# Optimization experiments

Hardware: AMD Instinct MI355X
Metric: run time of the kernel (lower is better)

The kernel has to match this reference:

```python
import jax, jax.numpy as jnp
import numpy as np

B, S, D, M = 8, 128, 512, 4
DEPTH, THR, TEMP, EPS = 16, 0.9999, 1.0, 1e-6


def setup_inputs() -> dict:
    key = jax.random.key(0)
    ks = jax.random.split(key, 13)
    def nrm(k, shape):
        return jax.random.normal(k, shape, jnp.float32) / np.sqrt(shape[-1]).astype(np.float32)
    return dict(
        x_real=jax.random.normal(ks[0], (B, S, D), jnp.float32),
        x_imag=jax.random.normal(ks[1], (B, S, D), jnp.float32),
        Wq_r=nrm(ks[2], (M, D, D)), Wq_i=nrm(ks[3], (M, D, D)),
        Wk_r=nrm(ks[4], (M, D, D)), Wk_i=nrm(ks[5], (M, D, D)),
        Wv_r=nrm(ks[6], (M, D, D)), Wv_i=nrm(ks[7], (M, D, D)),
        mod_bias=jnp.zeros((M, D), jnp.float32),
        ln_scale=jnp.ones((M, D), jnp.float32),
        ln_shift=jnp.zeros((M, D), jnp.float32),
        w_sal=nrm(ks[8], (M, 2 * D)),
        gru_Wih=nrm(ks[9], (2 * D, 3 * D)),
        gru_Whh=nrm(ks[10], (D, 3 * D)),
        gru_bih=jnp.zeros((3 * D,), jnp.float32),
        gru_bhh=jnp.zeros((3 * D,), jnp.float32),
        bias_W=nrm(ks[11], (D, M)),
        bias_b=jnp.zeros((M,), jnp.float32),
        w_halt=nrm(ks[12], (2 * D,)),
        b_halt=jnp.zeros((1,), jnp.float32),
    )


def reference(x_real, x_imag, Wq_r, Wq_i, Wk_r, Wk_i, Wv_r, Wv_i,
              mod_bias, ln_scale, ln_shift, w_sal,
              gru_Wih, gru_Whh, gru_bih, gru_bhh,
              bias_W, bias_b, w_halt, b_halt):
    scale = D ** -0.5

    def clin(xr, xi, Wr, Wi):
        # ComplexLinear broadcast over module axis: x [B,S,D], W [M,D,D] -> [M,B,S,D]
        rr = jnp.einsum('bsd,mde->mbse', xr, Wr)
        ii = jnp.einsum('bsd,mde->mbse', xi, Wi)
        ri = jnp.einsum('bsd,mde->mbse', xr, Wi)
        ir = jnp.einsum('bsd,mde->mbse', xi, Wr)
        return rr - ii, ri + ir

    def modules(zr, zi):
        # all M processor modules in parallel: ComplexAttention -> ModReLU -> ComplexLayerNorm
        qr, qi = clin(zr, zi, Wq_r, Wq_i)
        kr, ki = clin(zr, zi, Wk_r, Wk_i)
        vr, vi = clin(zr, zi, Wv_r, Wv_i)
        qf = jnp.concatenate([qr, qi], -1)            # [M,B,S,2D]
        kf = jnp.concatenate([kr, ki], -1)
        attn = jax.nn.softmax(jnp.einsum('mbsd,mbtd->mbst', qf, kf) * scale, -1)
        or_ = jnp.einsum('mbst,mbtd->mbsd', attn, vr)
        oi_ = jnp.einsum('mbst,mbtd->mbsd', attn, vi)
        # ModReLU
        mag = jnp.sqrt(or_ ** 2 + oi_ ** 2) + EPS
        g = jax.nn.relu(mag + mod_bias[:, None, None, :]) / mag
        or_, oi_ = or_ * g, oi_ * g
        # ComplexLayerNorm (normalize magnitude, keep phase; torch var is unbiased)
        mag = jnp.sqrt(or_ ** 2 + oi_ ** 2) + EPS
        mu = mag.mean(-1, keepdims=True)
        var = jnp.var(mag, axis=-1, keepdims=True, ddof=1)
        nm = (mag - mu) / jnp.sqrt(var + EPS)
        nm = nm * ln_scale[:, None, None, :] + ln_shift[:, None, None, :]
        ph = jnp.arctan2(oi_, or_)
        return nm * jnp.cos(ph), nm * jnp.sin(ph)

    def gru(xf, h):
        gx = xf @ gru_Wih + gru_bih
        gh = h @ gru_Whh + gru_bhh
        xr_, xz_, xn_ = jnp.split(gx, 3, -1)
        hr_, hz_, hn_ = jnp.split(gh, 3, -1)
        r = jax.nn.sigmoid(xr_ + hr_)
        zg = jax.nn.sigmoid(xz_ + hz_)
        n = jnp.tanh(xn_ + r * hn_)
        return (1.0 - zg) * n + zg * h

    def step(carry, _):
        zr, zi, h, cum, ar, ai, pond = carry
        pooled = jnp.concatenate([zr.mean(1), zi.mean(1)], -1)   # [B,2D]
        h = gru(pooled, h)                                       # ExecutiveController
        mbias = h @ bias_W + bias_b                              # [B,M]
        mr, mi = modules(zr, zi)                                 # [M,B,S,D]
        feat = jnp.concatenate([mr.mean(2), mi.mean(2)], -1)     # [M,B,2D]
        sal = jnp.einsum('mbf,mf->mb', feat, w_sal)              # salience
        w = jax.nn.softmax((sal + mbias.T) / TEMP, axis=0)       # module competition
        gr = jnp.einsum('mb,mbsd->bsd', w, mr)                   # global workspace broadcast
        gi = jnp.einsum('mb,mbsd->bsd', w, mi)
        gwp = jnp.concatenate([gr.mean(1), gi.mean(1)], -1)
        p = jax.nn.sigmoid(gwp @ w_halt + b_halt[0])             # [B] halting prob
        still = (cum < THR).astype(p.dtype)
        new_halt = ((cum + p) >= THR) & (cum < THR)
        wt = jnp.where(new_halt, 1.0 - cum, p) * still           # ACT weights
        cum = cum + wt
        ar = ar + wt[:, None, None] * gr
        ai = ai + wt[:, None, None] * gi
        pond = pond + still
        return (gr, gi, h, cum, ar, ai, pond), None

    z0 = jnp.zeros((B,), x_real.dtype)
    init = (x_real, x_imag, jnp.zeros((B, D), x_real.dtype), z0,
            jnp.zeros_like(x_real), jnp.zeros_like(x_imag), z0)
    (zr, zi, h, cum, ar, ai, pond), _ = jax.lax.scan(step, init, None, length=DEPTH)
    return jnp.stack([ar, ai])  # [2,B,S,D] accumulated workspace (real, imag)
```

## Files before the change

kernel.cpp:

```cpp
#include <hip/hip_runtime.h>
#include <math.h>

#define B 8
#define S 128
#define D 512
#define M 4
#define BS 1024
#define BSD 524288
#define DEPTH 16
#define THRESH 0.9999f
#define EPS 1e-6f
#define SCALE 0.04419417382415922f

typedef float floatx4 __attribute__((ext_vector_type(4)));
typedef short s8v __attribute__((ext_vector_type(8)));
typedef unsigned short us4 __attribute__((ext_vector_type(4)));

__device__ __forceinline__ unsigned short f2bf(float f) {
  unsigned int u = __float_as_uint(f);
  u += 0x7FFFu + ((u >> 16) & 1u);
  return (unsigned short)(u >> 16);
}
__device__ __forceinline__ float bf2f(unsigned short h) {
  return __uint_as_float((unsigned int)h << 16);
// ... 45 lines not shown
  ((float4*)(ws + OFF_ZI))[i4] = b;
  float4 z = {0.f, 0.f, 0.f, 0.f};
  ((float4*)(ws + OFF_AR))[i4] = z;
  ((float4*)(ws + OFF_AI))[i4] = z;
  int row = i4 >> 7;
  int d4 = (i4 & 127) * 4;
  float av[4] = {a.x, a.y, a.z, a.w}, bv[4] = {b.x, b.y, b.z, b.w};
  us4 hh, hl;
#pragma unroll
  for (int j = 0; j < 4; ++j) {
    unsigned short h = f2bf(av[j]); hh[j] = h; hl[j] = f2bf(av[j] - bf2f(h));
  }
  *(us4*)(xh + (size_t)row * 1024 + d4) = hh;
  *(us4*)(xl + (size_t)row * 1024 + d4) = hl;
#pragma unroll
  for (int j = 0; j < 4; ++j) {
    unsigned short h = f2bf(bv[j]); hh[j] = h; hl[j] = f2bf(bv[j] - bf2f(h));
  }
  *(us4*)(xh + (size_t)row * 1024 + 512 + d4) = hh;
  *(us4*)(xl + (size_t)row * 1024 + 512 + d4) = hl;
  if (i4 < (B * D) / 4) {
    ((float4*)(ws + OFF_H0))[i4] = z;
    ((float4*)(ws + OFF_H1))[i4] = z;
  }
  if (i4 < 16384) ((float4*)(ws + OFF_FEAT))[i4] = z;
  if (i4 < 2048)  ((float4*)(ws + OFF_GWP))[i4] = z;
  if (i4 < B) { ws[OFF_CUM + i4] = 0.f; ws[OFF_CUM2 + i4] = 0.f; }
}

__global__ __launch_bounds__(256) void k_wprep(const float* __restrict__ Wqr,
                                               const float* __restrict__ Wqi,
                                               const float* __restrict__ Wkr,
                                               const float* __restrict__ Wki,
                                               const float* __restrict__ Wvr,
                                               const float* __restrict__ Wvi,
                                               float* __restrict__ ws) {
  __shared__ float lt[64][65];
  unsigned short* wh = (unsigned short*)(ws + OFF_WH);
  unsigned short* wl = (unsigned short*)(ws + OFF_WL);
  int z = blockIdx.z, m = z / 6, idx = z % 6;
  const float* Wsrc;
  switch (idx) {
    case 0:  Wsrc = Wqr; break;
    case 1:  Wsrc = Wqi; break;
    case 2:  Wsrc = Wkr; break;
    case 3:  Wsrc = Wki; break;
    case 4:  Wsrc = Wvr; break;
    default: Wsrc = Wvi; break;
  }
  Wsrc += (size_t)m * D * D;
  int k0 = blockIdx.x * 64, n0 = blockIdx.y * 64;
  int tx = threadIdx.x & 63, ty = threadIdx.x >> 6;
#pragma unroll
  for (int i = 0; i < 16; ++i) {
    int kl = ty + i * 4;
    lt[kl][tx] = Wsrc[(size_t)(k0 + kl) * D + n0 + tx];
  }
  __syncthreads();
  unsigned short* whp = wh + (size_t)z * 262144;
  unsigned short* wlp = wl + (size_t)z * 262144;
#pragma unroll
  for (int i = 0; i < 16; ++i) {
    int nl = ty + i * 4;
    float v = lt[tx][nl];
    unsigned short h = f2bf(v);
    whp[(size_t)(n0 + nl) * 512 + k0 + tx] = h;
    wlp[(size_t)(n0 + nl) * 512 + k0 + tx] = f2bf(v - bf2f(h));
  }
}

__global__ __launch_bounds__(256) void k_gwp(const float* __restrict__ zr,
                                             const float* __restrict__ zi,
                                             float* __restrict__ gwp) {
  int idx = blockIdx.x * 256 + threadIdx.x;
  int b = idx >> 10;
  int f = idx & 1023;
  const float* src = (f < D) ? (zr + b * S * D + f) : (zi + b * S * D + (f - D));
  float s = 0.f;
#pragma unroll 8
  for (int ss = 0; ss < S; ++ss) s += src[ss * D];
  gwp[idx] = s * (1.0f / S);
}

__global__ __launch_bounds__(256) void k_qk(float* __restrict__ ws) {
  __shared__ __align__(16) unsigned short Ah[128 * 32], Al[128 * 32];
  __shared__ __align__(16) unsigned short Bh[128 * 32], Bl[128 * 32];
  int t = threadIdx.x;
  if (blockIdx.x == 0 && blockIdx.y == 0 && blockIdx.z == 0) {
    float4 z4 = {0.f, 0.f, 0.f, 0.f};
    for (int i = t; i < 4096; i += 256) ((float4*)(ws + OFF_PART))[i] = z4;
  }
  const unsigned short* xh = (const unsigned short*)(ws + OFF_XH);
  const unsigned short* xl = (const unsigned short*)(ws + OFF_XL);
  const unsigned short* wh = (const unsigned short*)(ws + OFF_WH);
  const unsigned short* wl = (const unsigned short*)(ws + OFF_WL);
  int z = blockIdx.z, m = z >> 2, w6 = z & 3;
  int pair = (w6 >> 1) * 2;
  int p1 = m * 6 + pair + (w6 & 1);
  int p2 = m * 6 + pair + ((w6 & 1) ^ 1);
  bool neg2 = ((w6 & 1) == 0);
  const unsigned short* PH1 = wh + (size_t)p1 * 262144;
  const unsigned short* PL1 = wl + (size_t)p1 * 262144;
  const unsigned short* PH2 = wh + (size_t)p2 * 262144;
  const unsigned short* PL2 = wl + (size_t)p2 * 262144;

  int row0 = blockIdx.y * 128;
  int col0 = blockIdx.x * 128;
  int lane = t & 63, w = t >> 6;
  int wr = w >> 1, wc = w & 1;
  int q = lane >> 4, r = lane & 15;
  int srow = t >> 2;
  int skoff = (t & 3) * 8;
  size_t wrow1 = (size_t)(col0 + srow) * 512 + skoff;
  size_t wrow2 = (size_t)(col0 + 64 + srow) * 512 + skoff;
  size_t xrow1 = (size_t)(row0 + srow) * 1024 + skoff;
  size_t xrow2 = (size_t)(row0 + 64 + srow) * 1024 + skoff;
  const s8v sgn = {(short)0x8000, (short)0x8000, (short)0x8000, (short)0x8000,
                   (short)0x8000, (short)0x8000, (short)0x8000, (short)0x8000};

  floatx4 acc[4][4];
#pragma unroll
  for (int i = 0; i < 4; ++i)
#pragma unroll
    for (int j = 0; j < 4; ++j) acc[i][j] = (floatx4){0.f, 0.f, 0.f, 0.f};

  for (int k0 = 0; k0 < 1024; k0 += 32) {
    const unsigned short *WgH, *WgL;
    int kk = k0;
    bool xon = false;
    if (k0 < 512) { WgH = PH1; WgL = PL1; }
    else          { WgH = PH2; WgL = PL2; kk = k0 - 512; xon = neg2; }
    gll16(xh + xrow1 + k0, (char*)Ah + t * 16);
    gll16(xh + xrow2 + k0, (char*)Ah + 4096 + t * 16);
    gll16(xl + xrow1 + k0, (char*)Al + t * 16);
    gll16(xl + xrow2 + k0, (char*)Al + 4096 + t * 16);
    gll16(WgH + wrow1 + kk, (char*)Bh + t * 16);
    gll16(WgH + wrow2 + kk, (char*)Bh + 4096 + t * 16);
    gll16(WgL + wrow1 + kk, (char*)Bl + t * 16);
    gll16(WgL + wrow2 + kk, (char*)Bl + 4096 + t * 16);
    __syncthreads();
    s8v ah[4], al[4], bh[4], bl[4];
#pragma unroll
    for (int i = 0; i < 4; ++i) {
      int ro = (wr * 64 + i * 16 + r) * 32 + q * 8;
      ah[i] = *(const s8v*)((const short*)Ah + ro);
      al[i] = *(const s8v*)((const short*)Al + ro);
    }
#pragma unroll
    for (int j = 0; j < 4; ++j) {
      int ro = (wc * 64 + j * 16 + r) * 32 + q * 8;
      bh[j] = *(const s8v*)((const short*)Bh + ro);
      bl[j] = *(const s8v*)((const short*)Bl + ro);
    }
    if (xon) {
#pragma unroll
      for (int j = 0; j < 4; ++j) { bh[j] = bh[j] ^ sgn; bl[j] = bl[j] ^ sgn; }
    }
#pragma unroll
    for (int i = 0; i < 4; ++i)
#pragma unroll
      for (int j = 0; j < 4; ++j) {
        acc[i][j] = __builtin_amdgcn_mfma_f32_16x16x32_bf16(ah[i], bh[j], acc[i][j], 0, 0, 0);
        acc[i][j] = __builtin_amdgcn_mfma_f32_16x16x32_bf16(ah[i], bl[j], acc[i][j], 0, 0, 0);
        acc[i][j] = __builtin_amdgcn_mfma_f32_16x16x32_bf16(al[i], bh[j], acc[i][j], 0, 0, 0);
      }
    __syncthreads();
  }
  unsigned short *dh, *dl;
  if (w6 < 2) { dh = (unsigned short*)(ws + OFF_QCH); dl = (unsigned short*)(ws + OFF_QCL); }
  else        { dh = (unsigned short*)(ws + OFF_KCH); dl = (unsigned short*)(ws + OFF_KCL); }
  int half = (w6 & 1) * 512;
  size_t base = (size_t)m * 1024 * 1024;
#pragma unroll
  for (int i = 0; i < 4; ++i)
#pragma unroll
    for (int j = 0; j < 4; ++j) {
      int rowb = row0 + wr * 64 + i * 16 + q * 4;
      int colb = col0 + wc * 64 + j * 16 + r;
#pragma unroll
      for (int reg = 0; reg < 4; ++reg) {
        float v = acc[i][j][reg];
        unsigned short h = f2bf(v);
        size_t idx = base + (size_t)(rowb + reg) * 1024 + half + colb;
        dh[idx] = h;
        dl[idx] = f2bf(v - bf2f(h));
      }
    }
}

__global__ __launch_bounds__(256) void k_vattn(float* __restrict__ ws,
                                               const float* __restrict__ gwp,
                                               const float* __restrict__ hold,
                                               const float* __restrict__ Wih,
                                               const float* __restrict__ Whh) {
  __shared__ __align__(16) unsigned short Ah[128 * 32], Al[128 * 32];
  __shared__ __align__(16) unsigned short Bh[128 * 32], Bl[128 * 32];
  __shared__ float rmax[64][4];
  __shared__ float rsum[64][4];
  int t = threadIdx.x;
  int blk = blockIdx.x;

  if (blk >= 320) {
    float* xbuf = (float*)Ah;
    float* hbuf = (float*)Al;
    float (*red)[64][4] = (float (*)[64][4])Bh;
    int idx = blk - 320;
    int b = idx >> 5;
    int cc = (idx >> 2) & 7;
    int kq = idx & 3;
    int c0 = cc * 64;
    int td = t & 63, ks = t >> 6;
    for (int f = t; f < 1024; f += 256) xbuf[f] = gwp[b * 1024 + f];
    for (int d2 = t; d2 < 512; d2 += 256) hbuf[d2] = hold[b * 512 + d2];
    __syncthreads();
    float aR = 0.f, aZ = 0.f, aXn = 0.f, aHn = 0.f;
    int kbeg = kq * 384 + ks * 96, kend = kbeg + 96;
#pragma unroll 8
    for (int kk = kbeg; kk < kend; ++kk) {
      bool ih = kk < 1024;
      float x = ih ? xbuf[kk] : hbuf[kk - 1024];
      const float* base = ih ? (Wih + (size_t)kk * 1536) : (Whh + (size_t)(kk - 1024) * 1536);
      float wr = base[c0 + td];
      float wz = base[512 + c0 + td];
      float wn = base[1024 + c0 + td];
      aR += x * wr;
      aZ += x * wz;
      if (ih) aXn += x * wn; else aHn += x * wn;
    }
    red[ks][td][0] = aR;
    red[ks][td][1] = aZ;
    red[ks][td][2] = aXn;
    red[ks][td][3] = aHn;
    __syncthreads();
    if (t < 64) {
      float r_ = 0.f, z_ = 0.f, xn = 0.f, hn = 0.f;
#pragma unroll
      for (int s = 0; s < 4; ++s) {
        r_ += red[s][t][0]; z_ += red[s][t][1]; xn += red[s][t][2]; hn += red[s][t][3];
      }
      float* part = ws + OFF_PART + ((size_t)b * 512 + c0 + t) * 4;
      atomicAdd(part + 0, r_);
      atomicAdd(part + 1, z_);
      atomicAdd(part + 2, xn);
      atomicAdd(part + 3, hn);
    }
    return;
  }

  if (blk >= 256) {
    const unsigned short* qch = (const unsigned short*)(ws + OFF_QCH);
    const unsigned short* qcl = (const unsigned short*)(ws + OFF_QCL);
    const unsigned short* kch = (const unsigned short*)(ws + OFF_KCH);
    const unsigned short* kcl = (const unsigned short*)(ws + OFF_KCL);
    unsigned short* ph = (unsigned short*)(ws + OFF_PH);
    unsigned short* pl = (unsigned short*)(ws + OFF_PL);
    int ablk = blk - 256, mb = ablk >> 1, half = ablk & 1;
    size_t gbase = (size_t)mb * 128 * 1024;
    int lane = t & 63, wc = t >> 6;
    int q = lane >> 4, r = lane & 15;
    int srow = t >> 2;
    int skoff = (t & 3) * 8;
    size_t arow = gbase + (size_t)(half * 64 + srow) * 1024 + skoff;
    size_t brow1 = gbase + (size_t)srow * 1024 + skoff;
    size_t brow2 = gbase + (size_t)(64 + srow) * 1024 + skoff;

    floatx4 acc[4][2];
#pragma unroll
    for (int i = 0; i < 4; ++i)
#pragma unroll
      for (int j = 0; j < 2; ++j) acc[i][j] = (floatx4){0.f, 0.f, 0.f, 0.f};

    for (int k0 = 0; k0 < 1024; k0 += 32) {
      gll16(qch + arow + k0, (char*)Ah + t * 16);
      gll16(qcl + arow + k0, (char*)Al + t * 16);
      gll16(kch + brow1 + k0, (char*)Bh + t * 16);
      gll16(kch + brow2 + k0, (char*)Bh + 4096 + t * 16);
      gll16(kcl + brow1 + k0, (char*)Bl + t * 16);
      gll16(kcl + brow2 + k0, (char*)Bl + 4096 + t * 16);
      __syncthreads();
      s8v ah[4], al[4], bh[2], bl[2];
#pragma unroll
      for (int i = 0; i < 4; ++i) {
        int ro = (i * 16 + r) * 32 + q * 8;
        ah[i] = *(const s8v*)((const short*)Ah + ro);
        al[i] = *(const s8v*)((const short*)Al + ro);
      }
#pragma unroll
      for (int j = 0; j < 2; ++j) {
        int ro = (wc * 32 + j * 16 + r) * 32 + q * 8;
        bh[j] = *(const s8v*)((const short*)Bh + ro);
        bl[j] = *(const s8v*)((const short*)Bl + ro);
      }
#pragma unroll
      for (int i = 0; i < 4; ++i)
#pragma unroll
        for (int j = 0; j < 2; ++j) {
          acc[i][j] = __builtin_amdgcn_mfma_f32_16x16x32_bf16(ah[i], bh[j], acc[i][j], 0, 0, 0);
          acc[i][j] = __builtin_amdgcn_mfma_f32_16x16x32_bf16(ah[i], bl[j], acc[i][j], 0, 0, 0);
          acc[i][j] = __builtin_amdgcn_mfma_f32_16x16x32_bf16(al[i], bh[j], acc[i][j], 0, 0, 0);
        }
      __syncthreads();
    }
#pragma unroll
    for (int i = 0; i < 4; ++i)
#pragma unroll
      for (int j = 0; j < 2; ++j)
#pragma unroll
        for (int reg = 0; reg < 4; ++reg) acc[i][j][reg] *= SCALE;
#pragma unroll
    for (int i = 0; i < 4; ++i)
#pragma unroll
      for (int reg = 0; reg < 4; ++reg) {
        float mx = fmaxf(acc[i][0][reg], acc[i][1][reg]);
        for (int o = 1; o < 16; o <<= 1) mx = fmaxf(mx, __shfl_xor(mx, o));
        if (r == 0) rmax[i * 16 + q * 4 + reg][wc] = mx;
      }
    __syncthreads();
#pragma unroll
    for (int i = 0; i < 4; ++i)
#pragma unroll
      for (int reg = 0; reg < 4; ++reg) {
        int row = i * 16 + q * 4 + reg;
        float gmx = fmaxf(fmaxf(rmax[row][0], rmax[row][1]),
                          fmaxf(rmax[row][2], rmax[row][3]));
        float sm = 0.f;
#pragma unroll
        for (int j = 0; j < 2; ++j) {
          float e = __expf(acc[i][j][reg] - gmx);
          acc[i][j][reg] = e;
          sm += e;
        }
        for (int o = 1; o < 16; o <<= 1) sm += __shfl_xor(sm, o);
        if (r == 0) rsum[row][wc] = sm;
      }
    __syncthreads();
#pragma unroll
    for (int i = 0; i < 4; ++i)
#pragma unroll
      for (int reg = 0; reg < 4; ++reg) {
        int row = i * 16 + q * 4 + reg;
        float inv = 1.f / (rsum[row][0] + rsum[row][1] + rsum[row][2] + rsum[row][3]);
        size_t rb = (size_t)(mb * 128 + half * 64 + row) * 128;
#pragma unroll
        for (int j = 0; j < 2; ++j) {
          float p = acc[i][j][reg] * inv;
          unsigned short h = f2bf(p);
          size_t idx = rb + wc * 32 + j * 16 + r;
          ph[idx] = h;
          pl[idx] = f2bf(p - bf2f(h));
        }
      }
    return;
  }

  const unsigned short* xh = (const unsigned short*)(ws + OFF_XH);
  const unsigned short* xl = (const unsigned short*)(ws + OFF_XL);
  const unsigned short* wh = (const unsigned short*)(ws + OFF_WH);
  const unsigned short* wl = (const unsigned short*)(ws + OFF_WL);
  int plane = blk >> 5, m = plane >> 1, w6 = 4 + (plane & 1);
  int bx = (blk & 31) >> 3, by = blk & 7;
  int p1 = m * 6 + 4 + (w6 & 1);
  int p2 = m * 6 + 4 + ((w6 & 1) ^ 1);
  bool neg2 = ((w6 & 1) == 0);
  const unsigned short* PH1 = wh + (size_t)p1 * 262144;
  const unsigned short* PL1 = wl + (size_t)p1 * 262144;
  const unsigned short* PH2 = wh + (size_t)p2 * 262144;
  const unsigned short* PL2 = wl + (size_t)p2 * 262144;

  int row0 = bx * 128;
  int col0 = by * 128;
  int lane = t & 63, w = t >> 6;
  int wr = w >> 1, wc = w & 1;
  int q = lane >> 4, r = lane & 15;
  int srow = t >> 2;
  int skoff = (t & 3) * 8;
  size_t wrow1 = (size_t)(row0 + srow) * 512 + skoff;
  size_t wrow2 = (size_t)(row0 + 64 + srow) * 512 + skoff;
  size_t xrow1 = (size_t)(col0 + srow) * 1024 + skoff;
  size_t xrow2 = (size_t)(col0 + 64 + srow) * 1024 + skoff;
  const s8v sgn = {(short)0x8000, (short)0x8000, (short)0x8000, (short)0x8000,
                   (short)0x8000, (short)0x8000, (short)0x8000, (short)0x8000};

  floatx4 acc[4][4];
#pragma unroll
  for (int i = 0; i < 4; ++i)
#pragma unroll
    for (int j = 0; j < 4; ++j) acc[i][j] = (floatx4){0.f, 0.f, 0.f, 0.f};

  for (int k0 = 0; k0 < 1024; k0 += 32) {
    const unsigned short *WgH, *WgL;
    int kk = k0;
    bool xon = false;
    if (k0 < 512) { WgH = PH1; WgL = PL1; }
    else          { WgH = PH2; WgL = PL2; kk = k0 - 512; xon = neg2; }
    gll16(WgH + wrow1 + kk, (char*)Ah + t * 16);
    gll16(WgH + wrow2 + kk, (char*)Ah + 4096 + t * 16);
    gll16(WgL + wrow1 + kk, (char*)Al + t * 16);
    gll16(WgL + wrow2 + kk, (char*)Al + 4096 + t * 16);
    gll16(xh + xrow1 + k0, (char*)Bh + t * 16);
    gll16(xh + xrow2 + k0, (char*)Bh + 4096 + t * 16);
    gll16(xl + xrow1 + k0, (char*)Bl + t * 16);
    gll16(xl + xrow2 + k0, (char*)Bl + 4096 + t * 16);
    __syncthreads();
    s8v ah[4], al[4], bh[4], bl[4];
#pragma unroll
    for (int i = 0; i < 4; ++i) {
      int ro = (wr * 64 + i * 16 + r) * 32 + q * 8;
      ah[i] = *(const s8v*)((const short*)Ah + ro);
      al[i] = *(const s8v*)((const short*)Al + ro);
    }
#pragma unroll
    for (int j = 0; j < 4; ++j) {
      int ro = (wc * 64 + j * 16 + r) * 32 + q * 8;
      bh[j] = *(const s8v*)((const short*)Bh + ro);
      bl[j] = *(const s8v*)((const short*)Bl + ro);
    }
    if (xon) {
#pragma unroll
      for (int i = 0; i < 4; ++i) { ah[i] = ah[i] ^ sgn; al[i] = al[i] ^ sgn; }
    }
#pragma unroll
    for (int i = 0; i < 4; ++i)
#pragma unroll
      for (int j = 0; j < 4; ++j) {
        acc[i][j] = __builtin_amdgcn_mfma_f32_16x16x32_bf16(ah[i], bh[j], acc[i][j], 0, 0, 0);
        acc[i][j] = __builtin_amdgcn_mfma_f32_16x16x32_bf16(ah[i], bl[j], acc[i][j], 0, 0, 0);
        acc[i][j] = __builtin_amdgcn_mfma_f32_16x16x32_bf16(al[i], bh[j], acc[i][j], 0, 0, 0);
      }
    __syncthreads();
  }
  unsigned short* dh = (unsigned short*)(ws + OFF_VTH);
  unsigned short* dl = (unsigned short*)(ws + OFF_VTL);
  size_t base = (size_t)((w6 & 1) * 4 + m) * 512 * 1024;
#pragma unroll
  for (int i = 0; i < 4; ++i)
#pragma unroll
    for (int j = 0; j < 4; ++j) {
      int rowb = row0 + wr * 64 + i * 16 + q * 4;
      int colb = col0 + wc * 64 + j * 16 + r;
#pragma unroll
      for (int reg = 0; reg < 4; ++reg) {
        float v = acc[i][j][reg];
        unsigned short h = f2bf(v);
        size_t idx = base + (size_t)(rowb + reg) * 1024 + colb;
        dh[idx] = h;
        dl[idx] = f2bf(v - bf2f(h));
      }
    }
}

__global__ __launch_bounds__(256) void k_pv(float* __restrict__ ws) {
  __shared__ __align__(16) unsigned short Ph_[64 * 32], Pl_[64 * 32];
  __shared__ __align__(16) unsigned short VrH[128 * 32], VrL[128 * 32];
  __shared__ __align__(16) unsigned short ViH[128 * 32], ViL[128 * 32];
  const unsigned short* ph = (const unsigned short*)(ws + OFF_PH);
  const unsigned short* pl = (const unsigned short*)(ws + OFF_PL);
  const unsigned short* vth = (const unsigned short*)(ws + OFF_VTH);
  const unsigned short* vtl = (const unsigned short*)(ws + OFF_VTL);
  int yb = blockIdx.y, mb = yb >> 1, half = yb & 1;
  int m = mb >> 3, b = mb & 7;
  int col0 = blockIdx.x * 128;
  int t = threadIdx.x, lane = t & 63, w = t >> 6;
  int wr = w >> 1, wc = w & 1;
  int q = lane >> 4, r = lane & 15;
  int srow = t >> 2;
  int skoff = (t & 3) * 8;
  size_t prow = (size_t)(mb * 128 + half * 64 + srow) * 128 + skoff;
  size_t vbr1 = ((size_t)(m * 512) + col0 + srow) * 1024 + b * 128 + skoff;
  size_t vbr2 = ((size_t)(m * 512) + col0 + 64 + srow) * 1024 + b * 128 + skoff;
  size_t vplane_i = (size_t)4 * 512 * 1024;

  floatx4 accR[2][4], accI[2][4];
#pragma unroll
  for (int i = 0; i < 2; ++i)
#pragma unroll
    for (int j = 0; j < 4; ++j) {
      accR[i][j] = (floatx4){0.f, 0.f, 0.f, 0.f};
      accI[i][j] = (floatx4){0.f, 0.f, 0.f, 0.f};
    }

  for (int k0 = 0; k0 < 128; k0 += 32) {
    gll16(ph + prow + k0, (char*)Ph_ + t * 16);
    gll16(pl + prow + k0, (char*)Pl_ + t * 16);
    gll16(vth + vbr1 + k0, (char*)VrH + t * 16);
    gll16(vth + vbr2 + k0, (char*)VrH + 4096 + t * 16);
    gll16(vtl + vbr1 + k0, (char*)VrL + t * 16);
    gll16(vtl + vbr2 + k0, (char*)VrL + 4096 + t * 16);
    gll16(vth + vplane_i + vbr1 + k0, (char*)ViH + t * 16);
    gll16(vth + vplane_i + vbr2 + k0, (char*)ViH + 4096 + t * 16);
    gll16(vtl + vplane_i + vbr1 + k0, (char*)ViL + t * 16);
    gll16(vtl + vplane_i + vbr2 + k0, (char*)ViL + 4096 + t * 16);
    __syncthreads();
    s8v ah[2], al[2];
#pragma unroll
    for (int i = 0; i < 2; ++i) {
      int ro = (wr * 32 + i * 16 + r) * 32 + q * 8;
      ah[i] = *(const s8v*)((const short*)Ph_ + ro);
      al[i] = *(const s8v*)((const short*)Pl_ + ro);
    }
#pragma unroll
    for (int j = 0; j < 4; ++j) {
      int ro = (wc * 64 + j * 16 + r) * 32 + q * 8;
      s8v vrh = *(const s8v*)((const short*)VrH + ro);
      s8v vrl = *(const s8v*)((const short*)VrL + ro);
      s8v vih = *(const s8v*)((const short*)ViH + ro);
      s8v vil = *(const s8v*)((const short*)ViL + ro);
#pragma unroll
      for (int i = 0; i < 2; ++i) {
        accR[i][j] = __builtin_amdgcn_mfma_f32_16x16x32_bf16(ah[i], vrh, accR[i][j], 0, 0, 0);
        accR[i][j] = __builtin_amdgcn_mfma_f32_16x16x32_bf16(ah[i], vrl, accR[i][j], 0, 0, 0);
        accR[i][j] = __builtin_amdgcn_mfma_f32_16x16x32_bf16(al[i], vrh, accR[i][j], 0, 0, 0);
        accI[i][j] = __builtin_amdgcn_mfma_f32_16x16x32_bf16(ah[i], vih, accI[i][j], 0, 0, 0);
        accI[i][j] = __builtin_amdgcn_mfma_f32_16x16x32_bf16(ah[i], vil, accI[i][j], 0, 0, 0);
        accI[i][j] = __builtin_amdgcn_mfma_f32_16x16x32_bf16(al[i], vih, accI[i][j], 0, 0, 0);
      }
    }
    __syncthreads();
  }
  float* orp = ws + OFF_OR + (size_t)mb * 128 * 512;
  float* oip = ws + OFF_OI + (size_t)mb * 128 * 512;
#pragma unroll
  for (int i = 0; i < 2; ++i)
#pragma unroll
    for (int j = 0; j < 4; ++j) {
      int rowb = half * 64 + wr * 32 + i * 16 + q * 4;
      int colb = col0 + wc * 64 + j * 16 + r;
#pragma unroll
      for (int reg = 0; reg < 4; ++reg) {
        orp[(size_t)(rowb + reg) * 512 + colb] = accR[i][j][reg];
// ... 187 lines not shown
  float w0 = ws[OFF_W + 0 * B + b], w1 = ws[OFF_W + 1 * B + b];
  float w2 = ws[OFF_W + 2 * B + b], w3 = ws[OFF_W + 3 * B + b];
  float wt = ws[OFF_WT + b];
  const float4* mr = (const float4*)(ws + OFF_OR);
  const float4* mi = (const float4*)(ws + OFF_OI);
  const int MS = BSD / 4;
  int row = i4 >> 7;
  int d4 = (i4 & 127) * 4;
  float4 r0 = mr[i4], r1 = mr[i4 + MS], r2 = mr[i4 + 2 * MS], r3 = mr[i4 + 3 * MS];
  float gvR[4];
  gvR[0] = w0 * r0.x + w1 * r1.x + w2 * r2.x + w3 * r3.x;
  gvR[1] = w0 * r0.y + w1 * r1.y + w2 * r2.y + w3 * r3.y;
  gvR[2] = w0 * r0.z + w1 * r1.z + w2 * r2.z + w3 * r3.z;
  gvR[3] = w0 * r0.w + w1 * r1.w + w2 * r2.w + w3 * r3.w;
  us4 hh, hl;
#pragma unroll
  for (int j = 0; j < 4; ++j) {
    unsigned short h = f2bf(gvR[j]); hh[j] = h; hl[j] = f2bf(gvR[j] - bf2f(h));
  }
  *(us4*)(xh + (size_t)row * 1024 + d4) = hh;
  *(us4*)(xl + (size_t)row * 1024 + d4) = hl;
  float4 s0 = mi[i4], s1 = mi[i4 + MS], s2 = mi[i4 + 2 * MS], s3 = mi[i4 + 3 * MS];
  float gvI[4];
  gvI[0] = w0 * s0.x + w1 * s1.x + w2 * s2.x + w3 * s3.x;
  gvI[1] = w0 * s0.y + w1 * s1.y + w2 * s2.y + w3 * s3.y;
  gvI[2] = w0 * s0.z + w1 * s1.z + w2 * s2.z + w3 * s3.z;
  gvI[3] = w0 * s0.w + w1 * s1.w + w2 * s2.w + w3 * s3.w;
#pragma unroll
  for (int j = 0; j < 4; ++j) {
    unsigned short h = f2bf(gvI[j]); hh[j] = h; hl[j] = f2bf(gvI[j] - bf2f(h));
  }
  *(us4*)(xh + (size_t)row * 1024 + 512 + d4) = hh;
  *(us4*)(xl + (size_t)row * 1024 + 512 + d4) = hl;
  float4 a = ((float4*)(ws + OFF_AR))[i4];
  a.x += wt * gvR[0]; a.y += wt * gvR[1]; a.z += wt * gvR[2]; a.w += wt * gvR[3];
  ((float4*)(ws + OFF_AR))[i4] = a;
  a = ((float4*)(ws + OFF_AI))[i4];
  a.x += wt * gvI[0]; a.y += wt * gvI[1]; a.z += wt * gvI[2]; a.w += wt * gvI[3];
  ((float4*)(ws + OFF_AI))[i4] = a;
}

__global__ __launch_bounds__(256) void k_out(const float* __restrict__ ws,
                                             float* __restrict__ out) {
  int i4 = blockIdx.x * 256 + threadIdx.x;
  ((float4*)out)[i4] = ((const float4*)(ws + OFF_AR))[i4];
  ((float4*)out)[i4 + BSD / 4] = ((const float4*)(ws + OFF_AI))[i4];
}

extern "C" void kernel_launch(void* const* d_in, const int* in_sizes, int n_in,
                              void* d_out, int out_size, void* d_ws, size_t ws_size,
                              hipStream_t stream) {
  (void)in_sizes; (void)n_in; (void)out_size; (void)ws_size;
  const float* x_real  = (const float*)d_in[0];
  const float* x_imag  = (const float*)d_in[1];
  const float* Wq_r    = (const float*)d_in[2];
  const float* Wq_i    = (const float*)d_in[3];
  const float* Wk_r    = (const float*)d_in[4];
  const float* Wk_i    = (const float*)d_in[5];
  const float* Wv_r    = (const float*)d_in[6];
  const float* Wv_i    = (const float*)d_in[7];
  const float* mod_bias = (const float*)d_in[8];
  const float* ln_scale = (const float*)d_in[9];
  const float* ln_shift = (const float*)d_in[10];
  const float* w_sal   = (const float*)d_in[11];
  const float* gru_Wih = (const float*)d_in[12];
  const float* gru_Whh = (const float*)d_in[13];
  const float* gru_bih = (const float*)d_in[14];
  const float* gru_bhh = (const float*)d_in[15];
  const float* bias_W  = (const float*)d_in[16];
  const float* bias_b  = (const float*)d_in[17];
  const float* w_halt  = (const float*)d_in[18];
  const float* b_halt  = (const float*)d_in[19];
  float* ws = (float*)d_ws;
  float* out = (float*)d_out;

  k_wprep<<<dim3(8, 8, 24), 256, 0, stream>>>(Wq_r, Wq_i, Wk_r, Wk_i, Wv_r, Wv_i, ws);
  k_init<<<512, 256, 0, stream>>>(x_real, x_imag, ws);
  k_gwp<<<32, 256, 0, stream>>>(ws + OFF_ZR, ws + OFF_ZI, ws + OFF_GWP);
  for (int step = 0; step < DEPTH; ++step) {
    const float* hold = ws + ((step & 1) ? OFF_H1 : OFF_H0);
    float* hnew = ws + ((step & 1) ? OFF_H0 : OFF_H1);
    const float* cumr = ws + ((step & 1) ? OFF_CUM2 : OFF_CUM);
    float* cumw = ws + ((step & 1) ? OFF_CUM : OFF_CUM2);
    k_qk<<<dim3(4, 8, 16), 256, 0, stream>>>(ws);
    k_vattn<<<576, 256, 0, stream>>>(ws, ws + OFF_GWP, hold, gru_Wih, gru_Whh);
    k_pv<<<dim3(4, 64), 256, 0, stream>>>(ws);
    k_modlnfeat<<<136, 256, 0, stream>>>(ws, mod_bias, ln_scale, ln_shift,
                                         hold, hnew, gru_bih, gru_bhh);
    k_wsel<<<1, 1024, 0, stream>>>(ws, hnew, bias_W, bias_b, w_sal,
                                   w_halt, b_halt, cumr, cumw);
    k_bcast<<<520, 256, 0, stream>>>(ws);
  }
  k_out<<<512, 256, 0, stream>>>(ws, out);
}
```

Measured before the change: 2.866 ms.

## Move V projection into QK projection kernel, pair attention softmax with GRU

The V-projection GEMM tiles move out of the attention/GRU kernel and into the Q/K projection launch, which grows from 16 to 24 z-slices. The second kernel now holds only the QK^T softmax blocks and the GRU matvec blocks. This balances work across the two launches: the projection kernel gets more blocks to fill the GPU, and the softmax kernel no longer waits behind the heavy V GEMM. The cost is branchy role selection inside the projection kernel, which may raise register pressure.

```diff
diff --git a/kernel.cpp b/kernel.cpp
--- a/kernel.cpp
+++ b/kernel.cpp
@@ -151,7 +151,7 @@
   gwp[idx] = s * (1.0f / S);
 }
 
-__global__ __launch_bounds__(256) void k_qk(float* __restrict__ ws) {
+__global__ __launch_bounds__(256) void k_qkv(float* __restrict__ ws) {
   __shared__ __align__(16) unsigned short Ah[128 * 32], Al[128 * 32];
   __shared__ __align__(16) unsigned short Bh[128 * 32], Bl[128 * 32];
   int t = threadIdx.x;
@@ -163,8 +163,12 @@
   const unsigned short* xl = (const unsigned short*)(ws + OFF_XL);
   const unsigned short* wh = (const unsigned short*)(ws + OFF_WH);
   const unsigned short* wl = (const unsigned short*)(ws + OFF_WL);
-  int z = blockIdx.z, m = z >> 2, w6 = z & 3;
-  int pair = (w6 >> 1) * 2;
+  int z = blockIdx.z;
+  bool qk = (z < 16);
+  int m, w6;
+  if (qk) { m = z >> 2; w6 = z & 3; }
+  else    { int plane = z - 16; m = plane >> 1; w6 = 4 + (plane & 1); }
+  int pair = qk ? ((w6 >> 1) * 2) : 4;
   int p1 = m * 6 + pair + (w6 & 1);
   int p2 = m * 6 + pair + ((w6 & 1) ^ 1);
   bool neg2 = ((w6 & 1) == 0);
@@ -173,17 +177,19 @@
   const unsigned short* PH2 = wh + (size_t)p2 * 262144;
   const unsigned short* PL2 = wl + (size_t)p2 * 262144;
 
-  int row0 = blockIdx.y * 128;
-  int col0 = blockIdx.x * 128;
+  int row0 = qk ? (blockIdx.y * 128) : (blockIdx.x * 128);
+  int col0 = qk ? (blockIdx.x * 128) : (blockIdx.y * 128);
+  int wb = qk ? col0 : row0;
+  int xb = qk ? row0 : col0;
   int lane = t & 63, w = t >> 6;
   int wr = w >> 1, wc = w & 1;
   int q = lane >> 4, r = lane & 15;
   int srow = t >> 2;
   int skoff = (t & 3) * 8;
-  size_t wrow1 = (size_t)(col0 + srow) * 512 + skoff;
-  size_t wrow2 = (size_t)(col0 + 64 + srow) * 512 + skoff;
-  size_t xrow1 = (size_t)(row0 + srow) * 1024 + skoff;
-  size_t xrow2 = (size_t)(row0 + 64 + srow) * 1024 + skoff;
+  size_t wrow1 = (size_t)(wb + srow) * 512 + skoff;
+  size_t wrow2 = (size_t)(wb + 64 + srow) * 512 + skoff;
+  size_t xrow1 = (size_t)(xb + srow) * 1024 + skoff;
+  size_t xrow2 = (size_t)(xb + 64 + srow) * 1024 + skoff;
   const s8v sgn = {(short)0x8000, (short)0x8000, (short)0x8000, (short)0x8000,
                    (short)0x8000, (short)0x8000, (short)0x8000, (short)0x8000};
 
@@ -199,14 +205,25 @@
     bool xon = false;
     if (k0 < 512) { WgH = PH1; WgL = PL1; }
     else          { WgH = PH2; WgL = PL2; kk = k0 - 512; xon = neg2; }
-    gll16(xh + xrow1 + k0, (char*)Ah + t * 16);
-    gll16(xh + xrow2 + k0, (char*)Ah + 4096 + t * 16);
-    gll16(xl + xrow1 + k0, (char*)Al + t * 16);
-    gll16(xl + xrow2 + k0, (char*)Al + 4096 + t * 16);
-    gll16(WgH + wrow1 + kk, (char*)Bh + t * 16);
-    gll16(WgH + wrow2 + kk, (char*)Bh + 4096 + t * 16);
-    gll16(WgL + wrow1 + kk, (char*)Bl + t * 16);
-    gll16(WgL + wrow2 + kk, (char*)Bl + 4096 + t * 16);
+    if (qk) {
+      gll16(xh + xrow1 + k0, (char*)Ah + t * 16);
+      gll16(xh + xrow2 + k0, (char*)Ah + 4096 + t * 16);
+      gll16(xl + xrow1 + k0, (char*)Al + t * 16);
+      gll16(xl + xrow2 + k0, (char*)Al + 4096 + t * 16);
+      gll16(WgH + wrow1 + kk, (char*)Bh + t * 16);
+      gll16(WgH + wrow2 + kk, (char*)Bh + 4096 + t * 16);
+      gll16(WgL + wrow1 + kk, (char*)Bl + t * 16);
+      gll16(WgL + wrow2 + kk, (char*)Bl + 4096 + t * 16);
+    } else {
+      gll16(WgH + wrow1 + kk, (char*)Ah + t * 16);
+      gll16(WgH + wrow2 + kk, (char*)Ah + 4096 + t * 16);
+      gll16(WgL + wrow1 + kk, (char*)Al + t * 16);
+      gll16(WgL + wrow2 + kk, (char*)Al + 4096 + t * 16);
+      gll16(xh + xrow1 + k0, (char*)Bh + t * 16);
+      gll16(xh + xrow2 + k0, (char*)Bh + 4096 + t * 16);
+      gll16(xl + xrow1 + k0, (char*)Bl + t * 16);
+      gll16(xl + xrow2 + k0, (char*)Bl + 4096 + t * 16);
+    }
     __syncthreads();
     s8v ah[4], al[4], bh[4], bl[4];
 #pragma unroll
@@ -222,8 +239,13 @@
       bl[j] = *(const s8v*)((const short*)Bl + ro);
     }
     if (xon) {
-#pragma unroll
-      for (int j = 0; j < 4; ++j) { bh[j] = bh[j] ^ sgn; bl[j] = bl[j] ^ sgn; }
+      if (qk) {
+#pragma unroll
+        for (int j = 0; j < 4; ++j) { bh[j] = bh[j] ^ sgn; bl[j] = bl[j] ^ sgn; }
+      } else {
+#pragma unroll
+        for (int i = 0; i < 4; ++i) { ah[i] = ah[i] ^ sgn; al[i] = al[i] ^ sgn; }
+      }
     }
 #pragma unroll
     for (int i = 0; i < 4; ++i)
@@ -236,10 +258,18 @@
     __syncthreads();
   }
   unsigned short *dh, *dl;
-  if (w6 < 2) { dh = (unsigned short*)(ws + OFF_QCH); dl = (unsigned short*)(ws + OFF_QCL); }
-  else        { dh = (unsigned short*)(ws + OFF_KCH); dl = (unsigned short*)(ws + OFF_KCL); }
-  int half = (w6 & 1) * 512;
-  size_t base = (size_t)m * 1024 * 1024;
+  size_t base;
+  int half = 0;
+  if (qk) {
+    if (w6 < 2) { dh = (unsigned short*)(ws + OFF_QCH); dl = (unsigned short*)(ws + OFF_QCL); }
+    else        { dh = (unsigned short*)(ws + OFF_KCH); dl = (unsigned short*)(ws + OFF_KCL); }
+    half = (w6 & 1) * 512;
+    base = (size_t)m * 1024 * 1024;
+  } else {
+    dh = (unsigned short*)(ws + OFF_VTH);
+    dl = (unsigned short*)(ws + OFF_VTL);
+    base = (size_t)((w6 & 1) * 4 + m) * 512 * 1024;
+  }
 #pragma unroll
   for (int i = 0; i < 4; ++i)
 #pragma unroll
@@ -257,11 +287,11 @@
     }
 }
 
-__global__ __launch_bounds__(256) void k_vattn(float* __restrict__ ws,
-                                               const float* __restrict__ gwp,
-                                               const float* __restrict__ hold,
-                                               const float* __restrict__ Wih,
-                                               const float* __restrict__ Whh) {
+__global__ __launch_bounds__(256) void k_attngru(float* __restrict__ ws,
+                                                 const float* __restrict__ gwp,
+                                                 const float* __restrict__ hold,
+                                                 const float* __restrict__ Wih,
+                                                 const float* __restrict__ Whh) {
   __shared__ __align__(16) unsigned short Ah[128 * 32], Al[128 * 32];
   __shared__ __align__(16) unsigned short Bh[128 * 32], Bl[128 * 32];
   __shared__ float rmax[64][4];
@@ -269,11 +299,11 @@
   int t = threadIdx.x;
   int blk = blockIdx.x;
 
-  if (blk >= 320) {
+  if (blk >= 64) {
     float* xbuf = (float*)Ah;
     float* hbuf = (float*)Al;
     float (*red)[64][4] = (float (*)[64][4])Bh;
-    int idx = blk - 320;
+    int idx = blk - 64;
     int b = idx >> 5;
     int cc = (idx >> 2) & 7;
     int kq = idx & 3;
@@ -316,204 +346,106 @@
     return;
   }
 
-  if (blk >= 256) {
-    const unsigned short* qch = (const unsigned short*)(ws + OFF_QCH);
-    const unsigned short* qcl = (const unsigned short*)(ws + OFF_QCL);
-    const unsigned short* kch = (const unsigned short*)(ws + OFF_KCH);
-    const unsigned short* kcl = (const unsigned short*)(ws + OFF_KCL);
-    unsigned short* ph = (unsigned short*)(ws + OFF_PH);
-    unsigned short* pl = (unsigned short*)(ws + OFF_PL);
-    int ablk = blk - 256, mb = ablk >> 1, half = ablk & 1;
-    size_t gbase = (size_t)mb * 128 * 1024;
-    int lane = t & 63, wc = t >> 6;
-    int q = lane >> 4, r = lane & 15;
-    int srow = t >> 2;
-    int skoff = (t & 3) * 8;
-    size_t arow = gbase + (size_t)(half * 64 + srow) * 1024 + skoff;
-    size_t brow1 = gbase + (size_t)srow * 1024 + skoff;
-    size_t brow2 = gbase + (size_t)(64 + srow) * 1024 + skoff;
-
-    floatx4 acc[4][2];
-#pragma unroll
-    for (int i = 0; i < 4; ++i)
-#pragma unroll
-      for (int j = 0; j < 2; ++j) acc[i][j] = (floatx4){0.f, 0.f, 0.f, 0.f};
-
-    for (int k0 = 0; k0 < 1024; k0 += 32) {
-      gll16(qch + arow + k0, (char*)Ah + t * 16);
-      gll16(qcl + arow + k0, (char*)Al + t * 16);
-      gll16(kch + brow1 + k0, (char*)Bh + t * 16);
-      gll16(kch + brow2 + k0, (char*)Bh + 4096 + t * 16);
-      gll16(kcl + brow1 + k0, (char*)Bl + t * 16);
-      gll16(kcl + brow2 + k0, (char*)Bl + 4096 + t * 16);
-      __syncthreads();
-      s8v ah[4], al[4], bh[2], bl[2];
-#pragma unroll
-      for (int i = 0; i < 4; ++i) {
-        int ro = (i * 16 + r) * 32 + q * 8;
-        ah[i] = *(const s8v*)((const short*)Ah + ro);
-        al[i] = *(const s8v*)((const short*)Al + ro);
-      }
-#pragma unroll
-      for (int j = 0; j < 2; ++j) {
-        int ro = (wc * 32 + j * 16 + r) * 32 + q * 8;
-        bh[j] = *(const s8v*)((const short*)Bh + ro);
-        bl[j] = *(const s8v*)((const short*)Bl + ro);
-      }
-#pragma unroll
-      for (int i = 0; i < 4; ++i)
-#pragma unroll
-        for (int j = 0; j < 2; ++j) {
-          acc[i][j] = __builtin_amdgcn_mfma_f32_16x16x32_bf16(ah[i], bh[j], acc[i][j], 0, 0, 0);
-          acc[i][j] = __builtin_amdgcn_mfma_f32_16x16x32_bf16(ah[i], bl[j], acc[i][j], 0, 0, 0);
-          acc[i][j] = __builtin_amdgcn_mfma_f32_16x16x32_bf16(al[i], bh[j], acc[i][j], 0, 0, 0);
-        }
-      __syncthreads();
-    }
-#pragma unroll
-    for (int i = 0; i < 4; ++i)
-#pragma unroll
-      for (int j = 0; j < 2; ++j)
-#pragma unroll
-        for (int reg = 0; reg < 4; ++reg) acc[i][j][reg] *= SCALE;
-#pragma unroll
-    for (int i = 0; i < 4; ++i)
-#pragma unroll
-      for (int reg = 0; reg < 4; ++reg) {
-        float mx = fmaxf(acc[i][0][reg], acc[i][1][reg]);
-        for (int o = 1; o < 16; o <<= 1) mx = fmaxf(mx, __shfl_xor(mx, o));
-        if (r == 0) rmax[i * 16 + q * 4 + reg][wc] = mx;
-      }
-    __syncthreads();
-#pragma unroll
-    for (int i = 0; i < 4; ++i)
-#pragma unroll
-      for (int reg = 0; reg < 4; ++reg) {
-        int row = i * 16 + q * 4 + reg;
-        float gmx = fmaxf(fmaxf(rmax[row][0], rmax[row][1]),
-                          fmaxf(rmax[row][2], rmax[row][3]));
-        float sm = 0.f;
-#pragma unroll
-        for (int j = 0; j < 2; ++j) {
-          float e = __expf(acc[i][j][reg] - gmx);
-          acc[i][j][reg] = e;
-          sm += e;
-        }
-        for (int o = 1; o < 16; o <<= 1) sm += __shfl_xor(sm, o);
-        if (r == 0) rsum[row][wc] = sm;
-      }
-    __syncthreads();
-#pragma unroll
-    for (int i = 0; i < 4; ++i)
-#pragma unroll
-      for (int reg = 0; reg < 4; ++reg) {
-        int row = i * 16 + q * 4 + reg;
-        float inv = 1.f / (rsum[row][0] + rsum[row][1] + rsum[row][2] + rsum[row][3]);
-        size_t rb = (size_t)(mb * 128 + half * 64 + row) * 128;
-#pragma unroll
-        for (int j = 0; j < 2; ++j) {
-          float p = acc[i][j][reg] * inv;
-          unsigned short h = f2bf(p);
-          size_t idx = rb + wc * 32 + j * 16 + r;
-          ph[idx] = h;
-          pl[idx] = f2bf(p - bf2f(h));
-        }
-      }
-    return;
-  }
-
-  const unsigned short* xh = (const unsigned short*)(ws + OFF_XH);
-  const unsigned short* xl = (const unsigned short*)(ws + OFF_XL);
-  const unsigned short* wh = (const unsigned short*)(ws + OFF_WH);
-  const unsigned short* wl = (const unsigned short*)(ws + OFF_WL);
-  int plane = blk >> 5, m = plane >> 1, w6 = 4 + (plane & 1);
-  int bx = (blk & 31) >> 3, by = blk & 7;
-  int p1 = m * 6 + 4 + (w6 & 1);
-  int p2 = m * 6 + 4 + ((w6 & 1) ^ 1);
-  bool neg2 = ((w6 & 1) == 0);
-  const unsigned short* PH1 = wh + (size_t)p1 * 262144;
-  const unsigned short* PL1 = wl + (size_t)p1 * 262144;
-  const unsigned short* PH2 = wh + (size_t)p2 * 262144;
-  const unsigned short* PL2 = wl + (size_t)p2 * 262144;
-
-  int row0 = bx * 128;
-  int col0 = by * 128;
-  int lane = t & 63, w = t >> 6;
-  int wr = w >> 1, wc = w & 1;
+  const unsigned short* qch = (const unsigned short*)(ws + OFF_QCH);
+  const unsigned short* qcl = (const unsigned short*)(ws + OFF_QCL);
+  const unsigned short* kch = (const unsigned short*)(ws + OFF_KCH);
+  const unsigned short* kcl = (const unsigned short*)(ws + OFF_KCL);
+  unsigned short* ph = (unsigned short*)(ws + OFF_PH);
+  unsigned short* pl = (unsigned short*)(ws + OFF_PL);
+  int mb = blk >> 1, half = blk & 1;
+  size_t gbase = (size_t)mb * 128 * 1024;
+  int lane = t & 63, wc = t >> 6;
   int q = lane >> 4, r = lane & 15;
   int srow = t >> 2;
   int skoff = (t & 3) * 8;
-  size_t wrow1 = (size_t)(row0 + srow) * 512 + skoff;
-  size_t wrow2 = (size_t)(row0 + 64 + srow) * 512 + skoff;
-  size_t xrow1 = (size_t)(col0 + srow) * 1024 + skoff;
-  size_t xrow2 = (size_t)(col0 + 64 + srow) * 1024 + skoff;
-  const s8v sgn = {(short)0x8000, (short)0x8000, (short)0x8000, (short)0x8000,
-                   (short)0x8000, (short)0x8000, (short)0x8000, (short)0x8000};
-
-  floatx4 acc[4][4];
+  size_t arow = gbase + (size_t)(half * 64 + srow) * 1024 + skoff;
+  size_t brow1 = gbase + (size_t)srow * 1024 + skoff;
+  size_t brow2 = gbase + (size_t)(64 + srow) * 1024 + skoff;
+
+  floatx4 acc[4][2];
 #pragma unroll
   for (int i = 0; i < 4; ++i)
 #pragma unroll
-    for (int j = 0; j < 4; ++j) acc[i][j] = (floatx4){0.f, 0.f, 0.f, 0.f};
+    for (int j = 0; j < 2; ++j) acc[i][j] = (floatx4){0.f, 0.f, 0.f, 0.f};
 
   for (int k0 = 0; k0 < 1024; k0 += 32) {
-    const unsigned short *WgH, *WgL;
-    int kk = k0;
-    bool xon = false;
-    if (k0 < 512) { WgH = PH1; WgL = PL1; }
-    else          { WgH = PH2; WgL = PL2; kk = k0 - 512; xon = neg2; }
-    gll16(WgH + wrow1 + kk, (char*)Ah + t * 16);
-    gll16(WgH + wrow2 + kk, (char*)Ah + 4096 + t * 16);
-    gll16(WgL + wrow1 + kk, (char*)Al + t * 16);
-    gll16(WgL + wrow2 + kk, (char*)Al + 4096 + t * 16);
-    gll16(xh + xrow1 + k0, (char*)Bh + t * 16);
-    gll16(xh + xrow2 + k0, (char*)Bh + 4096 + t * 16);
-    gll16(xl + xrow1 + k0, (char*)Bl + t * 16);
-    gll16(xl + xrow2 + k0, (char*)Bl + 4096 + t * 16);
+    gll16(qch + arow + k0, (char*)Ah + t * 16);
+    gll16(qcl + arow + k0, (char*)Al + t * 16);
+    gll16(kch + brow1 + k0, (char*)Bh + t * 16);
+    gll16(kch + brow2 + k0, (char*)Bh + 4096 + t * 16);
+    gll16(kcl + brow1 + k0, (char*)Bl + t * 16);
+    gll16(kcl + brow2 + k0, (char*)Bl + 4096 + t * 16);
     __syncthreads();
-    s8v ah[4], al[4], bh[4], bl[4];
+    s8v ah[4], al[4], bh[2], bl[2];
 #pragma unroll
     for (int i = 0; i < 4; ++i) {
-      int ro = (wr * 64 + i * 16 + r) * 32 + q * 8;
+      int ro = (i * 16 + r) * 32 + q * 8;
       ah[i] = *(const s8v*)((const short*)Ah + ro);
       al[i] = *(const s8v*)((const short*)Al + ro);
     }
 #pragma unroll
-    for (int j = 0; j < 4; ++j) {
-      int ro = (wc * 64 + j * 16 + r) * 32 + q * 8;
+    for (int j = 0; j < 2; ++j) {
+      int ro = (wc * 32 + j * 16 + r) * 32 + q * 8;
       bh[j] = *(const s8v*)((const short*)Bh + ro);
       bl[j] = *(const s8v*)((const short*)Bl + ro);
     }
-    if (xon) {
-#pragma unroll
-      for (int i = 0; i < 4; ++i) { ah[i] = ah[i] ^ sgn; al[i] = al[i] ^ sgn; }
-    }
 #pragma unroll
     for (int i = 0; i < 4; ++i)
 #pragma unroll
-      for (int j = 0; j < 4; ++j) {
+      for (int j = 0; j < 2; ++j) {
         acc[i][j] = __builtin_amdgcn_mfma_f32_16x16x32_bf16(ah[i], bh[j], acc[i][j], 0, 0, 0);
         acc[i][j] = __builtin_amdgcn_mfma_f32_16x16x32_bf16(ah[i], bl[j], acc[i][j], 0, 0, 0);
         acc[i][j] = __builtin_amdgcn_mfma_f32_16x16x32_bf16(al[i], bh[j], acc[i][j], 0, 0, 0);
       }
     __syncthreads();
   }
-  unsigned short* dh = (unsigned short*)(ws + OFF_VTH);
-  unsigned short* dl = (unsigned short*)(ws + OFF_VTL);
-  size_t base = (size_t)((w6 & 1) * 4 + m) * 512 * 1024;
 #pragma unroll
   for (int i = 0; i < 4; ++i)
 #pragma unroll
-    for (int j = 0; j < 4; ++j) {
-      int rowb = row0 + wr * 64 + i * 16 + q * 4;
-      int colb = col0 + wc * 64 + j * 16 + r;
-#pragma unroll
-      for (int reg = 0; reg < 4; ++reg) {
-        float v = acc[i][j][reg];
-        unsigned short h = f2bf(v);
-        size_t idx = base + (size_t)(rowb + reg) * 1024 + colb;
-        dh[idx] = h;
-        dl[idx] = f2bf(v - bf2f(h));
+    for (int j = 0; j < 2; ++j)
+#pragma unroll
+      for (int reg = 0; reg < 4; ++reg) acc[i][j][reg] *= SCALE;
+#pragma unroll
+  for (int i = 0; i < 4; ++i)
+#pragma unroll
+    for (int reg = 0; reg < 4; ++reg) {
+      float mx = fmaxf(acc[i][0][reg], acc[i][1][reg]);
+      for (int o = 1; o < 16; o <<= 1) mx = fmaxf(mx, __shfl_xor(mx, o));
+      if (r == 0) rmax[i * 16 + q * 4 + reg][wc] = mx;
+    }
+  __syncthreads();
+#pragma unroll
+  for (int i = 0; i < 4; ++i)
+#pragma unroll
+    for (int reg = 0; reg < 4; ++reg) {
+      int row = i * 16 + q * 4 + reg;
+      float gmx = fmaxf(fmaxf(rmax[row][0], rmax[row][1]),
+                        fmaxf(rmax[row][2], rmax[row][3]));
+      float sm = 0.f;
+#pragma unroll
+      for (int j = 0; j < 2; ++j) {
+        float e = __expf(acc[i][j][reg] - gmx);
+        acc[i][j][reg] = e;
+        sm += e;
+      }
+      for (int o = 1; o < 16; o <<= 1) sm += __shfl_xor(sm, o);
+      if (r == 0) rsum[row][wc] = sm;
+    }
+  __syncthreads();
+#pragma unroll
+  for (int i = 0; i < 4; ++i)
+#pragma unroll
+    for (int reg = 0; reg < 4; ++reg) {
+      int row = i * 16 + q * 4 + reg;
+      float inv = 1.f / (rsum[row][0] + rsum[row][1] + rsum[row][2] + rsum[row][3]);
+      size_t rb = (size_t)(mb * 128 + half * 64 + row) * 128;
+#pragma unroll
+      for (int j = 0; j < 2; ++j) {
+        float p = acc[i][j][reg] * inv;
+        unsigned short h = f2bf(p);
+        size_t idx = rb + wc * 32 + j * 16 + r;
+        ph[idx] = h;
+        pl[idx] = f2bf(p - bf2f(h));
       }
     }
 }
@@ -867,8 +799,8 @@
     float* hnew = ws + ((step & 1) ? OFF_H0 : OFF_H1);
     const float* cumr = ws + ((step & 1) ? OFF_CUM2 : OFF_CUM);
     float* cumw = ws + ((step & 1) ? OFF_CUM : OFF_CUM2);
-    k_qk<<<dim3(4, 8, 16), 256, 0, stream>>>(ws);
-    k_vattn<<<576, 256, 0, stream>>>(ws, ws + OFF_GWP, hold, gru_Wih, gru_Whh);
+    k_qkv<<<dim3(4, 8, 24), 256, 0, stream>>>(ws);
+    k_attngru<<<320, 256, 0, stream>>>(ws, ws + OFF_GWP, hold, gru_Wih, gru_Whh);
     k_pv<<<dim3(4, 64), 256, 0, stream>>>(ws);
     k_modlnfeat<<<136, 256, 0, stream>>>(ws, mod_bias, ln_scale, ln_shift,
                                          hold, hnew, gru_bih, gru_bhh);
```

Result: slower. 3.198 ms (+11.6%).
